# Optimization experiments

Hardware: AMD Instinct MI355X
Metric: run time of the kernel (lower is better)

Reference implementation:

```python
import jax, jax.numpy as jnp
import numpy as np

P = 0.3            # swap probability (matches init_kwargs p)
H = 224
W = 224
PERM_SEED = 42     # fixed key so the reference is deterministic


def _index_permute(key, h, w, p):
    """Sequential random-neighbor swap permutation over an h*w grid.

    Faithful to CLOPLayer._index_permute: visit all flat indices in a random
    order; for each, with prob p swap it with one of its 4 toroidal neighbors
    (each with prob p/4). Implemented as a lax.scan over the visitation order
    (the swaps are inherently sequential / order-dependent).
    """
    n = h * w
    k1, k2 = jax.random.split(key)
    order = jax.random.permutation(k1, n)                       # visitation order
    probs = jnp.array([1.0 - p, p / 4, p / 4, p / 4, p / 4], dtype=jnp.float32)
    rs = jax.random.choice(k2, 5, shape=(n,), p=probs)          # move type per step

    def step(indexes, inp):
        idx, r = inp
        i = idx // w
        j = idx % w
        ip = jnp.where(r == 1, (i + 1) % h, jnp.where(r == 2, (i - 1) % h, i))
        jp = jnp.where(r == 3, (j + 1) % w, jnp.where(r == 4, (j - 1) % w, j))
        idx2 = jnp.where(r == 0, idx, ip * w + jp)              # r==0 -> self-swap (no-op)
        a = indexes[idx]
        b = indexes[idx2]
        indexes = indexes.at[idx].set(b).at[idx2].set(a)
        return indexes, None

    indexes = jnp.arange(n, dtype=jnp.int32)
    indexes, _ = jax.lax.scan(step, indexes, (order.astype(jnp.int32), rs.astype(jnp.int32)))
    return indexes


def setup_inputs() -> dict:
    key = jax.random.key(0)
    x = jax.random.normal(key, (128, 3, H, W), dtype=jnp.float32)
    return {"x": x}


def reference(x) -> jnp.ndarray:
    b, c, h, w = x.shape
    idx = _index_permute(jax.random.key(PERM_SEED), h, w, P)     # [h*w] int32
    flat = x.reshape(b, c, h * w)
    # torch.gather(flat, 2, idx broadcast over b,c) == take along last axis
    res = jnp.take(flat, idx, axis=2)
    return res.reshape(b, c, h, w)
```

## Files before the change

kernel.cpp:

```cpp
#include <hip/hip_runtime.h>
#include <cstdint>
#include <cstring>
#include <vector>
#include <algorithm>


#define PH 224
#define PW 224
#define PN (PH * PW)
#define NBC (128 * 3)

#define R_OUT 32
#define HALO 8
#define S_ROWS (R_OUT + 2 * HALO)
#define NWIN (PH / R_OUT)
#define KWIN (R_OUT * PW)
#define TPB 512
#define STAGE_F4 (S_ROWS * (PW / 4))
#define EMIT_F4 (KWIN / 4)

typedef float f4v __attribute__((ext_vector_type(4)));
typedef unsigned short u4v __attribute__((ext_vector_type(4)));

static inline uint32_t rotl32(uint32_t v, int d) {
  return (v << d) | (v >> (32 - d));
}

static void tf2x32(uint32_t k0, uint32_t k1, uint32_t x0, uint32_t x1,
                   uint32_t& o0, uint32_t& o1) {
  const uint32_t ks0 = k0, ks1 = k1, ks2 = k0 ^ k1 ^ 0x1BD11BDAu;
  uint32_t v0 = x0 + ks0;
  uint32_t v1 = x1 + ks1;
  static const int ra[4] = {13, 15, 26, 6};
  static const int rb[4] = {17, 29, 16, 24};
#define R4X(rr)                             \
  do {                                      \
    for (int _i = 0; _i < 4; ++_i) {        \
      v0 += v1;                             \
      v1 = rotl32(v1, (rr)[_i]);            \
      v1 ^= v0;                             \
    }                                       \
  } while (0)
  R4X(ra); v0 += ks1; v1 += ks2 + 1u;
  R4X(rb); v0 += ks2; v1 += ks0 + 2u;
  R4X(ra); v0 += ks0; v1 += ks1 + 3u;
  R4X(rb); v0 += ks1; v1 += ks2 + 4u;
  R4X(ra); v0 += ks2; v1 += ks0 + 5u;
#undef R4X
  o0 = v0;
  o1 = v1;
}

static void jax_split2(uint32_t k0, uint32_t k1,
                       uint32_t& a0, uint32_t& a1, uint32_t& b0, uint32_t& b1) {
  tf2x32(k0, k1, 0u, 0u, a0, a1);
  tf2x32(k0, k1, 0u, 1u, b0, b1);
}

static inline uint32_t jax_rb32(uint32_t k0, uint32_t k1, uint32_t i) {
  uint32_t y0, y1;
  tf2x32(k0, k1, 0u, i, y0, y1);
  return y0 ^ y1;
}

static std::vector<int> compute_perm() {
  const int n = PN;
  const uint32_t K0 = 0u, K1 = 42u;

  uint32_t k1a, k1b, k2a, k2b;
  jax_split2(K0, K1, k1a, k1b, k2a, k2b);

  std::vector<int> order(n);
  for (int i = 0; i < n; ++i) order[i] = i;
  uint32_t ck0 = k1a, ck1 = k1b;
  std::vector<std::pair<uint32_t, int>> kv(n);
  for (int round = 0; round < 2; ++round) {
    uint32_t nk0, nk1, sk0, sk1;
    jax_split2(ck0, ck1, nk0, nk1, sk0, sk1);
    ck0 = nk0; ck1 = nk1;
    for (int i = 0; i < n; ++i) {
      kv[i] = {jax_rb32(sk0, sk1, (uint32_t)i), order[i]};
    }
    std::stable_sort(kv.begin(), kv.end(),
                     [](const std::pair<uint32_t, int>& a,
                        const std::pair<uint32_t, int>& b) {
                       return a.first < b.first;
                     });
    for (int i = 0; i < n; ++i) order[i] = kv[i].second;
  }

  float probs[5] = {(float)(1.0 - 0.3), (float)(0.3 / 4), (float)(0.3 / 4),
                    (float)(0.3 / 4), (float)(0.3 / 4)};
  float pc[5];
  pc[0] = probs[0];
  for (int i = 1; i < 5; ++i) pc[i] = pc[i - 1] + probs[i];

  std::vector<uint8_t> rs(n);
  for (int i = 0; i < n; ++i) {
    uint32_t bits = jax_rb32(k2a, k2b, (uint32_t)i);
    uint32_t fb = (bits >> 9) | 0x3f800000u;
    float u;
    std::memcpy(&u, &fb, 4);
    u -= 1.0f;
    if (u < 0.0f) u = 0.0f;
    float r = pc[4] * (1.0f - u);
    int ind = (int)(std::lower_bound(pc, pc + 5, r) - pc);
    rs[i] = (uint8_t)ind;
  }

  std::vector<int> idx(n);
  for (int i = 0; i < n; ++i) idx[i] = i;
  for (int t = 0; t < n; ++t) {
    const int id = order[t];
    const int r = rs[t];
    const int i = id / PW, j = id % PW;
    int ip = i, jp = j;
    if (r == 1)      ip = (i + 1) % PH;
    else if (r == 2) ip = (i - 1 + PH) % PH;
    else if (r == 3) jp = (j + 1) % PW;
    else if (r == 4) jp = (j - 1 + PW) % PW;
    const int id2 = (r == 0) ? id : (ip * PW + jp);
    const int a = idx[id];
    const int b = idx[id2];
    idx[id]  = b;
    idx[id2] = a;
  }
  return idx;
}

struct PermHolder {
  std::vector<int> h_idx;
  std::vector<uint16_t> h_lofs;
  int* d_idx = nullptr;
  uint16_t* d_lofs = nullptr;
  bool lds_ok = false;

  PermHolder() {
    h_idx = compute_perm();

    h_lofs.assign((size_t)NWIN * KWIN, 0);
    bool ok = true;
    for (int w = 0; w < NWIN && ok; ++w) {
      const int g0 = w * R_OUT - HALO;
      for (int kk = 0; kk < KWIN; ++kk) {
        const int k = w * KWIN + kk;
        const int s = h_idx[k];
        const int srow = s / PW, scol = s % PW;
        int i = ((srow - g0) % PH + PH) % PH;
        if (i >= S_ROWS) { ok = false; break; }
        h_lofs[(size_t)w * KWIN + kk] = (uint16_t)(i * PW + scol);
      }
    }

    int* p = nullptr;
    if (hipMalloc(&p, PN * sizeof(int)) == hipSuccess &&
        hipMemcpy(p, h_idx.data(), PN * sizeof(int),
                  hipMemcpyHostToDevice) == hipSuccess) {
      d_idx = p;
    }
    if (ok) {
      uint16_t* q = nullptr;
      if (hipMalloc(&q, (size_t)NWIN * KWIN * sizeof(uint16_t)) == hipSuccess &&
          hipMemcpy(q, h_lofs.data(), (size_t)NWIN * KWIN * sizeof(uint16_t),
                    hipMemcpyHostToDevice) == hipSuccess) {
        d_lofs = q;
        lds_ok = true;
      }
    }
  }
};
static PermHolder g_perm;

__global__ __launch_bounds__(TPB) void clop_lds(
    const float* __restrict__ x, const uint16_t* __restrict__ lofs,
    float* __restrict__ out) {
  __shared__ float tile[S_ROWS * PW];

  const int w = blockIdx.x;
  const size_t bc = blockIdx.y;
  const int g0 = w * R_OUT - HALO;
  const float* xs = x + bc * PN;

  const uint16_t* lw = lofs + (size_t)w * KWIN;
  u4v o4[4];
#pragma unroll
  for (int i = 0; i < 4; ++i) {
    const int t = (int)threadIdx.x + i * TPB;
    if (t < EMIT_F4) o4[i] = *(const u4v*)(lw + t * 4);
  }

#pragma unroll
  for (int i = 0; i < 6; ++i) {
    const int t = (int)threadIdx.x + i * TPB;
    if (t < STAGE_F4) {
      const int r = t / (PW / 4);
      const int j = (t % (PW / 4)) * 4;
      int g = g0 + r;
      if (g < 0) g += PH;
      else if (g >= PH) g -= PH;
      *(f4v*)(tile + r * PW + j) = *(const f4v*)(xs + g * PW + j);
    }
  }
  __syncthreads();

  float* ob = out + bc * PN + (size_t)w * KWIN;
#pragma unroll
  for (int i = 0; i < 4; ++i) {
    const int t = (int)threadIdx.x + i * TPB;
    if (t < EMIT_F4) {
      f4v v;
      v.x = tile[o4[i].x];
      v.y = tile[o4[i].y];
      v.z = tile[o4[i].z];
      v.w = tile[o4[i].w];
      __builtin_nontemporal_store(v, (f4v*)(ob + t * 4));
    }
  }
}

__global__ __launch_bounds__(256) void clop_gather(
    const float* __restrict__ x, const int* __restrict__ idx,
    float* __restrict__ out) {
  const int k = blockIdx.x * 256 + threadIdx.x;
  const int s = idx[k];
  const size_t bc0 = (size_t)blockIdx.y * 8;
#pragma unroll
  for (int t = 0; t < 8; ++t) {
    const size_t bc = bc0 + t;
    out[bc * PN + k] = x[bc * PN + s];
  }
}

extern "C" void kernel_launch(void* const* d_in, const int* in_sizes, int n_in,
                              void* d_out, int out_size, void* d_ws,
                              size_t ws_size, hipStream_t stream) {
  const float* x = (const float*)d_in[0];
  float* out = (float*)d_out;

  if (g_perm.lds_ok) {
    dim3 grid(NWIN, NBC);
    clop_lds<<<grid, TPB, 0, stream>>>(x, g_perm.d_lofs, out);
    return;
  }

  const int* idx;
  if (g_perm.d_idx != nullptr) {
    idx = g_perm.d_idx;
  } else {
    (void)hipMemcpyAsync(d_ws, g_perm.h_idx.data(), PN * sizeof(int),
                         hipMemcpyHostToDevice, stream);
    idx = (const int*)d_ws;
  }
  dim3 grid(PN / 256, NBC / 8);
  clop_gather<<<grid, 256, 0, stream>>>(x, idx, out);
}
```

Measured before the change: 135.4 us.

## Shrink LDS halo with overflow list for out-of-window gather sources

Lets the LDS-staged gather use a 2-row halo instead of 8. Any source pixel that falls outside the smaller window is recorded in a per-window overflow list, loaded by scalar global reads into extra LDS slots, and its offset is redirected to that slot. The goal is to cut redundant halo reads (48 down to 36 staged rows per 32 output rows) and shrink LDS use so more blocks fit per CU; launch bounds now request 8 blocks. In exchange it adds scattered overflow loads and a counter read per block.

```diff
diff --git a/kernel.cpp b/kernel.cpp
--- a/kernel.cpp
+++ b/kernel.cpp
@@ -11,13 +11,11 @@
 #define NBC (128 * 3)
 
 #define R_OUT 32
-#define HALO 8
-#define S_ROWS (R_OUT + 2 * HALO)
 #define NWIN (PH / R_OUT)
 #define KWIN (R_OUT * PW)
 #define TPB 512
-#define STAGE_F4 (S_ROWS * (PW / 4))
 #define EMIT_F4 (KWIN / 4)
+#define OVF_CAP 1024
 
 typedef float f4v __attribute__((ext_vector_type(4)));
 typedef unsigned short u4v __attribute__((ext_vector_type(4)));
@@ -128,29 +126,45 @@
   return idx;
 }
 
+static bool build_tables(const std::vector<int>& idx, int halo,
+                         std::vector<uint16_t>& lofs, std::vector<int>& ovf,
+                         std::vector<int>& cnt) {
+  const int sr = R_OUT + 2 * halo;
+  lofs.assign((size_t)NWIN * KWIN, 0);
+  ovf.assign((size_t)NWIN * OVF_CAP, 0);
+  cnt.assign(NWIN, 0);
+  for (int w = 0; w < NWIN; ++w) {
+    const int g0 = w * R_OUT - halo;
+    int no = 0;
+    for (int kk = 0; kk < KWIN; ++kk) {
+      const int k = w * KWIN + kk;
+      const int s = idx[k];
+      const int srow = s / PW, scol = s % PW;
+      int i = ((srow - g0) % PH + PH) % PH;
+      if (i < sr) {
+        lofs[(size_t)w * KWIN + kk] = (uint16_t)(i * PW + scol);
+      } else {
+        if (no >= OVF_CAP) return false;
+        ovf[(size_t)w * OVF_CAP + no] = s;
+        lofs[(size_t)w * KWIN + kk] = (uint16_t)(sr * PW + no);
+        ++no;
+      }
+    }
+    cnt[w] = no;
+  }
+  return true;
+}
+
 struct PermHolder {
   std::vector<int> h_idx;
-  std::vector<uint16_t> h_lofs;
   int* d_idx = nullptr;
   uint16_t* d_lofs = nullptr;
-  bool lds_ok = false;
+  int* d_ovf = nullptr;
+  int* d_cnt = nullptr;
+  int halo = 0;
 
   PermHolder() {
     h_idx = compute_perm();
-
-    h_lofs.assign((size_t)NWIN * KWIN, 0);
-    bool ok = true;
-    for (int w = 0; w < NWIN && ok; ++w) {
-      const int g0 = w * R_OUT - HALO;
-      for (int kk = 0; kk < KWIN; ++kk) {
-        const int k = w * KWIN + kk;
-        const int s = h_idx[k];
-        const int srow = s / PW, scol = s % PW;
-        int i = ((srow - g0) % PH + PH) % PH;
-        if (i >= S_ROWS) { ok = false; break; }
-        h_lofs[(size_t)w * KWIN + kk] = (uint16_t)(i * PW + scol);
-      }
-    }
 
     int* p = nullptr;
     if (hipMalloc(&p, PN * sizeof(int)) == hipSuccess &&
@@ -158,27 +172,49 @@
                   hipMemcpyHostToDevice) == hipSuccess) {
       d_idx = p;
     }
-    if (ok) {
-      uint16_t* q = nullptr;
-      if (hipMalloc(&q, (size_t)NWIN * KWIN * sizeof(uint16_t)) == hipSuccess &&
-          hipMemcpy(q, h_lofs.data(), (size_t)NWIN * KWIN * sizeof(uint16_t),
-                    hipMemcpyHostToDevice) == hipSuccess) {
-        d_lofs = q;
-        lds_ok = true;
+
+    for (int h : {2, 8}) {
+      std::vector<uint16_t> lofs;
+      std::vector<int> ovf, cnt;
+      if (!build_tables(h_idx, h, lofs, ovf, cnt)) continue;
+      uint16_t* ql = nullptr;
+      int* qo = nullptr;
+      int* qc = nullptr;
+      bool ok =
+          hipMalloc(&ql, lofs.size() * sizeof(uint16_t)) == hipSuccess &&
+          hipMemcpy(ql, lofs.data(), lofs.size() * sizeof(uint16_t),
+                    hipMemcpyHostToDevice) == hipSuccess &&
+          hipMalloc(&qo, ovf.size() * sizeof(int)) == hipSuccess &&
+          hipMemcpy(qo, ovf.data(), ovf.size() * sizeof(int),
+                    hipMemcpyHostToDevice) == hipSuccess &&
+          hipMalloc(&qc, cnt.size() * sizeof(int)) == hipSuccess &&
+          hipMemcpy(qc, cnt.data(), cnt.size() * sizeof(int),
+                    hipMemcpyHostToDevice) == hipSuccess;
+      if (ok) {
+        d_lofs = ql;
+        d_ovf = qo;
+        d_cnt = qc;
+        halo = h;
+        break;
       }
     }
   }
 };
 static PermHolder g_perm;
 
-__global__ __launch_bounds__(TPB) void clop_lds(
+template <int HALO_T>
+__global__ __launch_bounds__(TPB, 8) void clop_lds_t(
     const float* __restrict__ x, const uint16_t* __restrict__ lofs,
+    const int* __restrict__ ovf_idx, const int* __restrict__ ovf_cnt,
     float* __restrict__ out) {
-  __shared__ float tile[S_ROWS * PW];
+  constexpr int SR = R_OUT + 2 * HALO_T;
+  constexpr int STAGE = SR * (PW / 4);
+  constexpr int SITER = (STAGE + TPB - 1) / TPB;
+  __shared__ float tile[SR * PW + OVF_CAP];
 
   const int w = blockIdx.x;
   const size_t bc = blockIdx.y;
-  const int g0 = w * R_OUT - HALO;
+  const int g0 = w * R_OUT - HALO_T;
   const float* xs = x + bc * PN;
 
   const uint16_t* lw = lofs + (size_t)w * KWIN;
@@ -189,10 +225,14 @@
     if (t < EMIT_F4) o4[i] = *(const u4v*)(lw + t * 4);
   }
 
+  const int novf = ovf_cnt[w];
+  for (int t = (int)threadIdx.x; t < novf; t += TPB)
+    tile[SR * PW + t] = xs[ovf_idx[w * OVF_CAP + t]];
+
 #pragma unroll
-  for (int i = 0; i < 6; ++i) {
+  for (int i = 0; i < SITER; ++i) {
     const int t = (int)threadIdx.x + i * TPB;
-    if (t < STAGE_F4) {
+    if (t < STAGE) {
       const int r = t / (PW / 4);
       const int j = (t % (PW / 4)) * 4;
       int g = g0 + r;
@@ -237,9 +277,16 @@
   const float* x = (const float*)d_in[0];
   float* out = (float*)d_out;
 
-  if (g_perm.lds_ok) {
+  if (g_perm.halo == 2) {
     dim3 grid(NWIN, NBC);
-    clop_lds<<<grid, TPB, 0, stream>>>(x, g_perm.d_lofs, out);
+    clop_lds_t<2><<<grid, TPB, 0, stream>>>(x, g_perm.d_lofs, g_perm.d_ovf,
+                                            g_perm.d_cnt, out);
+    return;
+  }
+  if (g_perm.halo == 8) {
+    dim3 grid(NWIN, NBC);
+    clop_lds_t<8><<<grid, TPB, 0, stream>>>(x, g_perm.d_lofs, g_perm.d_ovf,
+                                            g_perm.d_cnt, out);
     return;
   }
 
```

After: 136.0 us. About the same (+0.5%).

## Replace LDS-staged window gather with direct vectorized global gather

Applied to the files above, without the earlier changes.

Removes the shared-memory staging path, which loaded a 48-row halo window per 32-row output window and read source elements from LDS. Each block now covers one seventh of a channel plane, reads four int32 indices at a time and gathers straight from global memory, depending on L2/L1 locality, then writes float4 with nontemporal stores. This drops the halo re-reads, the LDS footprint and the barrier. In exchange it issues scattered global loads and reads 4-byte indices instead of 2-byte ones.

```diff
diff --git a/kernel.cpp b/kernel.cpp
--- a/kernel.cpp
+++ b/kernel.cpp
@@ -10,17 +10,12 @@
 #define PN (PH * PW)
 #define NBC (128 * 3)
 
-#define R_OUT 32
-#define HALO 8
-#define S_ROWS (R_OUT + 2 * HALO)
-#define NWIN (PH / R_OUT)
-#define KWIN (R_OUT * PW)
-#define TPB 512
-#define STAGE_F4 (S_ROWS * (PW / 4))
-#define EMIT_F4 (KWIN / 4)
+#define NWIN 7
+#define KWIN (PN / NWIN)
+#define GTPB 256
+#define GIT (KWIN / 4 / GTPB)
 
 typedef float f4v __attribute__((ext_vector_type(4)));
-typedef unsigned short u4v __attribute__((ext_vector_type(4)));
 
 static inline uint32_t rotl32(uint32_t v, int d) {
   return (v << d) | (v >> (32 - d));
@@ -130,104 +125,40 @@
 
 struct PermHolder {
   std::vector<int> h_idx;
-  std::vector<uint16_t> h_lofs;
   int* d_idx = nullptr;
-  uint16_t* d_lofs = nullptr;
-  bool lds_ok = false;
 
   PermHolder() {
     h_idx = compute_perm();
-
-    h_lofs.assign((size_t)NWIN * KWIN, 0);
-    bool ok = true;
-    for (int w = 0; w < NWIN && ok; ++w) {
-      const int g0 = w * R_OUT - HALO;
-      for (int kk = 0; kk < KWIN; ++kk) {
-        const int k = w * KWIN + kk;
-        const int s = h_idx[k];
-        const int srow = s / PW, scol = s % PW;
-        int i = ((srow - g0) % PH + PH) % PH;
-        if (i >= S_ROWS) { ok = false; break; }
-        h_lofs[(size_t)w * KWIN + kk] = (uint16_t)(i * PW + scol);
-      }
-    }
-
     int* p = nullptr;
     if (hipMalloc(&p, PN * sizeof(int)) == hipSuccess &&
         hipMemcpy(p, h_idx.data(), PN * sizeof(int),
                   hipMemcpyHostToDevice) == hipSuccess) {
       d_idx = p;
     }
-    if (ok) {
-      uint16_t* q = nullptr;
-      if (hipMalloc(&q, (size_t)NWIN * KWIN * sizeof(uint16_t)) == hipSuccess &&
-          hipMemcpy(q, h_lofs.data(), (size_t)NWIN * KWIN * sizeof(uint16_t),
-                    hipMemcpyHostToDevice) == hipSuccess) {
-        d_lofs = q;
-        lds_ok = true;
-      }
-    }
   }
 };
 static PermHolder g_perm;
 
-__global__ __launch_bounds__(TPB) void clop_lds(
-    const float* __restrict__ x, const uint16_t* __restrict__ lofs,
+__global__ __launch_bounds__(GTPB) void clop_gather4(
+    const float* __restrict__ x, const int* __restrict__ idx,
     float* __restrict__ out) {
-  __shared__ float tile[S_ROWS * PW];
-
   const int w = blockIdx.x;
   const size_t bc = blockIdx.y;
-  const int g0 = w * R_OUT - HALO;
+  const int base = w * KWIN;
   const float* xs = x + bc * PN;
-
-  const uint16_t* lw = lofs + (size_t)w * KWIN;
-  u4v o4[4];
-#pragma unroll
-  for (int i = 0; i < 4; ++i) {
-    const int t = (int)threadIdx.x + i * TPB;
-    if (t < EMIT_F4) o4[i] = *(const u4v*)(lw + t * 4);
-  }
+  float* ob = out + bc * PN + base;
+  const int4* iv = (const int4*)(idx + base);
 
 #pragma unroll
-  for (int i = 0; i < 6; ++i) {
-    const int t = (int)threadIdx.x + i * TPB;
-    if (t < STAGE_F4) {
-      const int r = t / (PW / 4);
-      const int j = (t % (PW / 4)) * 4;
-      int g = g0 + r;
-      if (g < 0) g += PH;
-      else if (g >= PH) g -= PH;
-      *(f4v*)(tile + r * PW + j) = *(const f4v*)(xs + g * PW + j);
-    }
-  }
-  __syncthreads();
-
-  float* ob = out + bc * PN + (size_t)w * KWIN;
-#pragma unroll
-  for (int i = 0; i < 4; ++i) {
-    const int t = (int)threadIdx.x + i * TPB;
-    if (t < EMIT_F4) {
-      f4v v;
-      v.x = tile[o4[i].x];
-      v.y = tile[o4[i].y];
-      v.z = tile[o4[i].z];
-      v.w = tile[o4[i].w];
-      __builtin_nontemporal_store(v, (f4v*)(ob + t * 4));
-    }
-  }
-}
-
-__global__ __launch_bounds__(256) void clop_gather(
-    const float* __restrict__ x, const int* __restrict__ idx,
-    float* __restrict__ out) {
-  const int k = blockIdx.x * 256 + threadIdx.x;
-  const int s = idx[k];
-  const size_t bc0 = (size_t)blockIdx.y * 8;
-#pragma unroll
-  for (int t = 0; t < 8; ++t) {
-    const size_t bc = bc0 + t;
-    out[bc * PN + k] = x[bc * PN + s];
+  for (int i = 0; i < GIT; ++i) {
+    const int g = i * GTPB + (int)threadIdx.x;
+    const int4 s = iv[g];
+    f4v v;
+    v.x = xs[s.x];
+    v.y = xs[s.y];
+    v.z = xs[s.z];
+    v.w = xs[s.w];
+    __builtin_nontemporal_store(v, (f4v*)(ob + (size_t)g * 4));
   }
 }
 
@@ -237,12 +168,6 @@
   const float* x = (const float*)d_in[0];
   float* out = (float*)d_out;
 
-  if (g_perm.lds_ok) {
-    dim3 grid(NWIN, NBC);
-    clop_lds<<<grid, TPB, 0, stream>>>(x, g_perm.d_lofs, out);
-    return;
-  }
-
   const int* idx;
   if (g_perm.d_idx != nullptr) {
     idx = g_perm.d_idx;
@@ -251,6 +176,7 @@
                          hipMemcpyHostToDevice, stream);
     idx = (const int*)d_ws;
   }
-  dim3 grid(PN / 256, NBC / 8);
-  clop_gather<<<grid, 256, 0, stream>>>(x, idx, out);
+
+  dim3 grid(NWIN, NBC);
+  clop_gather4<<<grid, GTPB, 0, stream>>>(x, idx, out);
 }
```

New measurement: 146.0 us. 1.08x slower.
